# Performance work log

Hardware: AMD Instinct MI355X
Metric: run time of the kernel (lower is better)

## Reference

```python
import jax, jax.numpy as jnp
import numpy as np
from jax import lax

B, N, E, H = 512, 128, 256, 8
D = E // H
CLIP = 10.0
NEG = -1e9  # finite stand-in for -inf (backward-safe, math-identical after softmax)


def setup_inputs() -> dict:
    key = jax.random.key(0)
    ks = jax.random.split(key, 5)
    s = lambda k, shape: jax.random.normal(k, shape, jnp.float32) * 0.05
    return {
        "node_embeddings": jax.random.normal(ks[0], (B, N, E), jnp.float32),
        "Wqkv": s(ks[1], (E, 3 * E)), "bqkv": jnp.zeros((3 * E,), jnp.float32),
        "Wfix": s(ks[2], (E, E)), "bfix": jnp.zeros((E,), jnp.float32),
        "Wstep": s(ks[3], (2 * E, E)), "bstep": jnp.zeros((E,), jnp.float32),
        "Wmlp": s(ks[4], (E, E)), "bmlp": jnp.zeros((E,), jnp.float32),
    }


def reference(node_embeddings, Wqkv, bqkv, Wfix, bfix, Wstep, bstep, Wmlp, bmlp):
    scale = 1.0 / np.sqrt(D)
    graph_emb = node_embeddings.mean(axis=1)                       # (B,E)
    qkv = node_embeddings @ Wqkv + bqkv                            # (B,N,3E)
    k, v, logit_k = jnp.split(qkv, 3, axis=-1)
    kh = k.reshape(B, N, H, D).transpose(0, 2, 1, 3)               # (B,H,N,D)
    vh = v.reshape(B, N, H, D).transpose(0, 2, 1, 3)               # (B,H,N,D)
    fixed = graph_emb @ Wfix + bfix                                # (B,E)
    first = node_embeddings[:, 0, :]                               # (B,E)
    bidx = jnp.arange(B)

    def step(carry, _):
        current, visited, logp_sum = carry
        last = node_embeddings[bidx, current]                      # gather last action emb (B,E)
        q = fixed + (jnp.concatenate([first, last], axis=-1) @ Wstep + bstep)
        qh = q.reshape(B, H, D)                                    # single query per head
        attn = jnp.einsum('bhd,bhnd->bhn', qh, kh) * scale
        attn = jnp.where(visited[:, None, :], NEG, attn)
        attn = jax.nn.softmax(attn, axis=-1)
        ctx = jnp.einsum('bhn,bhnd->bhd', attn, vh).reshape(B, E)
        x = ctx @ Wmlp + bmlp                                      # (B,E)
        logits = jnp.einsum('be,bne->bn', x, logit_k) * scale      # (B,N)
        logits = jnp.tanh(logits) * CLIP
        logits = jnp.where(visited, NEG, logits)
        log_p = jax.nn.log_softmax(logits, axis=-1)
        action = jnp.argmax(log_p, axis=-1)                        # greedy decode
        chosen = jnp.take_along_axis(log_p, action[:, None], axis=1)[:, 0]
        visited = visited | jax.nn.one_hot(action, N, dtype=bool)
        return (action, visited, logp_sum + chosen), action

    visited0 = jnp.zeros((B, N), bool).at[:, 0].set(True)
    current0 = jnp.zeros((B,), jnp.int32)
    (_, _, logp_sum), seq = lax.scan(
        step, (current0, visited0, jnp.zeros((B,), jnp.float32)), None, length=N - 1)
    return logp_sum                                                # (B,) summed log-prob of tour
```

## Files before the change

kernel.cpp:

```cpp
#include <hip/hip_runtime.h>
#include <math.h>


#define B_ 512
#define N_ 128
#define E_ 256
#define H_ 8
#define D_ 32
#define NEG (-1.0e9f)
#define CLIPV 10.0f
#define SCALE 0.17677669529663688110f

template <int CTRL>
__device__ __forceinline__ float dpp_f(float x) {
  int r = __builtin_amdgcn_update_dpp(__float_as_int(x), __float_as_int(x),
                                      CTRL, 0xf, 0xf, false);
  return __int_as_float(r);
}
__device__ __forceinline__ float wred_max(float v) {
  v = fmaxf(v, dpp_f<0xB1>(v));
  v = fmaxf(v, dpp_f<0x4E>(v));
  v = fmaxf(v, dpp_f<0x124>(v));
  v = fmaxf(v, dpp_f<0x128>(v));
  v = fmaxf(v, __shfl_xor(v, 16));
  v = fmaxf(v, __shfl_xor(v, 32));
  return v;
}
__device__ __forceinline__ float wred_sum(float v) {
  v += dpp_f<0xB1>(v);
  v += dpp_f<0x4E>(v);
  v += dpp_f<0x124>(v);
  v += dpp_f<0x128>(v);
  v += __shfl_xor(v, 16);
  v += __shfl_xor(v, 32);
  return v;
}

__global__ void k0_prep(const float* __restrict__ Wqkv, const float* __restrict__ bqkv,
                        const float* __restrict__ Wmlp, const float* __restrict__ bmlp,
                        float* __restrict__ Wc, float* __restrict__ bc,
                        float* __restrict__ wc2, float* __restrict__ cconst) {
  int t = threadIdx.x;
  int blk = blockIdx.x;
  __shared__ float row_s[E_];
  if (blk < E_) {
    int g = blk;
    row_s[t] = Wqkv[g * 768 + 512 + t];
    __syncthreads();
    int f = t;
    const float4* wm4 = (const float4*)(Wmlp + f * E_);
    const float4* w34 = (const float4*)row_s;
    float acc = 0.f;
#pragma unroll 8
    for (int j = 0; j < E_ / 4; ++j) {
      float4 a = w34[j]; float4 bv = wm4[j];
      acc += a.x * bv.x + a.y * bv.y + a.z * bv.z + a.w * bv.w;
    }
    Wc[g * E_ + f] = acc;
  } else {
    int f = t;
    float a1 = 0.f, a2 = 0.f;
    for (int e = 0; e < E_; ++e) {
      a1 += bqkv[512 + e] * Wmlp[f * E_ + e];
      a2 += Wqkv[f * 768 + 512 + e] * bmlp[e];
    }
    bc[f] = a1;
    wc2[f] = a2;
    if (t == 0) {
      float c = 0.f;
      for (int e = 0; e < E_; ++e) c += bqkv[512 + e] * bmlp[e];
      *cconst = c;
    }
  }
}

__global__ __launch_bounds__(256, 2)
void k_gemm(const float* __restrict__ emb, const float* __restrict__ Wqkv,
            const float* __restrict__ bqkv,
            const float* __restrict__ Wc, const float* __restrict__ bc,
            float* __restrict__ kk_, float* __restrict__ vv_,
            float* __restrict__ lk2, int ncc, int tmask) {
  __shared__ float As[256 * 64];
  int t = threadIdx.x;
  int r0 = blockIdx.x * 64;
  {
    int m = t >> 2;
    int c0 = t & 3;
    const float4* e4 = (const float4*)emb;
#pragma unroll
    for (int p = 0; p < 16; ++p) {
      int c4 = c0 + p * 4;
      float4 a = e4[(size_t)(r0 + m) * 64 + c4];
      As[(c4 * 4 + 0) * 64 + m] = a.x;
      As[(c4 * 4 + 1) * 64 + m] = a.y;
      As[(c4 * 4 + 2) * 64 + m] = a.z;
      As[(c4 * 4 + 3) * 64 + m] = a.w;
    }
  }
  __syncthreads();
  int tx = t & 15, ty = t >> 4;
  const float4* As4 = (const float4*)As;
  for (int cc = 0; cc < ncc; ++cc) {
    const float* Bp; int ldb4; const float* bias; float* outp;
    int colbase = (cc & 1) * 128;
    switch (cc >> 1) {
      case 0:  Bp = Wqkv + colbase;          ldb4 = 192; bias = bqkv + colbase;       outp = kk_; break;
      case 1:  Bp = Wqkv + 256 + colbase;    ldb4 = 192; bias = bqkv + 256 + colbase; outp = vv_; break;
      default: Bp = Wc + colbase;            ldb4 = 64;  bias = bc + colbase;         outp = lk2; break;
    }
    const float4* B4 = (const float4*)Bp;
    float acc[4][8];
#pragma unroll
    for (int i = 0; i < 4; ++i)
#pragma unroll
      for (int j = 0; j < 8; ++j) acc[i][j] = 0.f;

#pragma unroll 4
    for (int kk = 0; kk < 256; ++kk) {
      float4 b0 = B4[kk * ldb4 + tx * 2];
      float4 b1 = B4[kk * ldb4 + tx * 2 + 1];
      float4 av = As4[kk * 16 + ty];
      float a_[4] = {av.x, av.y, av.z, av.w};
#pragma unroll
      for (int i = 0; i < 4; ++i) {
        acc[i][0] += a_[i] * b0.x; acc[i][1] += a_[i] * b0.y;
        acc[i][2] += a_[i] * b0.z; acc[i][3] += a_[i] * b0.w;
        acc[i][4] += a_[i] * b1.x; acc[i][5] += a_[i] * b1.y;
        acc[i][6] += a_[i] * b1.z; acc[i][7] += a_[i] * b1.w;
      }
    }
    float bj[8];
#pragma unroll
    for (int j = 0; j < 8; ++j) bj[j] = bias ? bias[tx * 8 + j] : 0.f;
    int tr = (tmask >> (cc >> 1)) & 1;
    if (!tr) {
#pragma unroll
      for (int i = 0; i < 4; ++i) {
        int row = r0 + ty * 4 + i;
        float4 o0 = make_float4(acc[i][0] + bj[0], acc[i][1] + bj[1], acc[i][2] + bj[2], acc[i][3] + bj[3]);
        float4 o1 = make_float4(acc[i][4] + bj[4], acc[i][5] + bj[5], acc[i][6] + bj[6], acc[i][7] + bj[7]);
        float4* o4 = (float4*)(outp + (size_t)row * 256 + colbase + tx * 8);
        o4[0] = o0; o4[1] = o1;
      }
    } else {
#pragma unroll
      for (int i = 0; i < 4; ++i) {
        int row = r0 + ty * 4 + i;
        int bb = row >> 7, nn = row & 127;
        float* op = outp + (size_t)bb * 32768 + nn;
#pragma unroll
        for (int j = 0; j < 8; ++j)
          op[(size_t)(colbase + tx * 8 + j) * 128] = acc[i][j] + bj[j];
      }
    }
  }
}

__global__ void k_qbase(const float* __restrict__ emb, const float* __restrict__ Wfix,
                        const float* __restrict__ bfix, const float* __restrict__ Wstep,
                        const float* __restrict__ bstep, float* __restrict__ qbase) {
  int b = blockIdx.x, t = threadIdx.x;
  __shared__ float ge[E_], fi[E_];
  const float* eb = emb + (size_t)b * N_ * E_;
  float s = 0.f;
#pragma unroll 8
  for (int n = 0; n < N_; ++n) s += eb[n * E_ + t];
  ge[t] = s * (1.0f / 128.0f);
  fi[t] = eb[t];
  __syncthreads();
  float acc = bfix[t] + bstep[t];
#pragma unroll 4
  for (int g = 0; g < E_; ++g)
    acc += ge[g] * Wfix[g * E_ + t] + fi[g] * Wstep[g * E_ + t];
  qbase[b * E_ + t] = acc;
}

__global__ void k_c(const float* __restrict__ emb, const float* __restrict__ wc2,
                    const float* __restrict__ cconst, float* __restrict__ cvec) {
  __shared__ float w[E_];
  int t = threadIdx.x;
  w[t] = wc2[t];
  __syncthreads();
  int row = blockIdx.x * 256 + t;
  const float4* e4 = (const float4*)(emb + (size_t)row * E_);
  const float4* w4 = (const float4*)w;
  float acc = 0.f;
#pragma unroll 8
  for (int j = 0; j < E_ / 4; ++j) {
    float4 a = e4[j], bv = w4[j];
    acc += a.x * bv.x + a.y * bv.y + a.z * bv.z + a.w * bv.w;
  }
  cvec[row] = acc + *cconst;
}

__global__ __launch_bounds__(512) __attribute__((amdgpu_waves_per_eu(2, 2)))
void k_roll(const float* __restrict__ emb, const float* __restrict__ Wstep,
            const float* __restrict__ kT, const float* __restrict__ vv_,
            const float* __restrict__ lkT,
            const float* __restrict__ qbase, const float* __restrict__ cvec,
            float* __restrict__ out) {
  int lt = threadIdx.x;
  int b = blockIdx.x;
  int h = lt >> 6;
  int j = lt & 63;

  __shared__ float sq_lds[128 * 260];
  __shared__ float work[6144];
  float* at_s  = work;
  float* ctx_s = work + 1024;
  float* zp    = work + 1280;

  {
    float* At = work;
    float* Bs = work + 2048;
    const float4* eb4 = (const float4*)(emb + (size_t)b * 32768);
    const float* W2 = Wstep + 65536;
    int n0 = (lt & 31) * 4;
    int e0 = (lt >> 5) * 16;
    float acc[4][16];
#pragma unroll
    for (int i = 0; i < 4; ++i)
#pragma unroll
      for (int jj = 0; jj < 16; ++jj) acc[i][jj] = 0.f;

    for (int gc = 0; gc < 16; ++gc) {
      {
        int n = lt & 127, q4g = lt >> 7;
        float4 a = eb4[n * 64 + gc * 4 + q4g];
        At[(q4g * 4 + 0) * 128 + n] = a.x;
        At[(q4g * 4 + 1) * 128 + n] = a.y;
        At[(q4g * 4 + 2) * 128 + n] = a.z;
        At[(q4g * 4 + 3) * 128 + n] = a.w;
      }
      {
        const float4* w4 = (const float4*)(W2 + gc * 16 * 256);
        ((float4*)Bs)[lt] = w4[lt];
        ((float4*)Bs)[lt + 512] = w4[lt + 512];
      }
      __syncthreads();
#pragma unroll
      for (int gi = 0; gi < 16; ++gi) {
        float4 a4 = *(const float4*)(At + gi * 128 + n0);
        const float4* bp = (const float4*)(Bs + gi * 256 + e0);
        float4 b0 = bp[0], b1 = bp[1], b2 = bp[2], b3 = bp[3];
        float av[4] = {a4.x, a4.y, a4.z, a4.w};
        float bv[16] = {b0.x, b0.y, b0.z, b0.w, b1.x, b1.y, b1.z, b1.w,
                        b2.x, b2.y, b2.z, b2.w, b3.x, b3.y, b3.z, b3.w};
#pragma unroll
        for (int i = 0; i < 4; ++i)
#pragma unroll
          for (int jj = 0; jj < 16; ++jj) acc[i][jj] += av[i] * bv[jj];
      }
      __syncthreads();
    }
    const float* qb = qbase + (size_t)b * 256;
    float qbr[16];
#pragma unroll
    for (int jj = 0; jj < 16; ++jj) qbr[jj] = qb[e0 + jj];
#pragma unroll
    for (int i = 0; i < 4; ++i)
#pragma unroll
      for (int jj = 0; jj < 16; ++jj)
        sq_lds[(n0 + i) * 260 + e0 + jj] = acc[i][jj] + qbr[jj];
  }
  __syncthreads();
  __builtin_amdgcn_sched_barrier(0);

  const float* kTb = kT + (size_t)b * 32768;
  const float* vb  = vv_ + (size_t)b * 32768;
  const float* lTb = lkT + (size_t)b * 32768;

  float k0r[32], k1r[32];
#pragma unroll
  for (int d = 0; d < 32; ++d) {
    k0r[d] = kTb[(h * 32 + d) * 128 + j];
    k1r[d] = kTb[(h * 32 + d) * 128 + j + 64];
  }
  int e_own = h * 32 + (j & 31), nh = j >> 5;
  float vr[64];
#pragma unroll
  for (int m = 0; m < 64; ++m) vr[m] = vb[(nh * 64 + m) * 256 + e_own];
  float l0r[32], l1r[32];
#pragma unroll
  for (int e = 0; e < 32; ++e) {
    l0r[e] = lTb[(h * 32 + e) * 128 + j];
    l1r[e] = lTb[(h * 32 + e) * 128 + j + 64];
  }
  float cv_lo = cvec[b * 128 + j];
  float cv_hi = cvec[b * 128 + j + 64];
  int vis_lo = (j == 0) ? 1 : 0, vis_hi = 0;
  int cur = 0;
  float lp = 0.f;

#pragma unroll 1
  for (int it = 0; it < N_ - 1; ++it) {
    const float4* q4 = (const float4*)(sq_lds + cur * 260 + h * 32);
    float sa0 = 0.f, sb0 = 0.f, sa1 = 0.f, sb1 = 0.f;
#pragma unroll
    for (int dd = 0; dd < 8; ++dd) {
      float4 qv = q4[dd];
      if (dd & 1) {
        sb0 += qv.x * k0r[dd * 4] + qv.y * k0r[dd * 4 + 1] + qv.z * k0r[dd * 4 + 2] + qv.w * k0r[dd * 4 + 3];
        sb1 += qv.x * k1r[dd * 4] + qv.y * k1r[dd * 4 + 1] + qv.z * k1r[dd * 4 + 2] + qv.w * k1r[dd * 4 + 3];
      } else {
        sa0 += qv.x * k0r[dd * 4] + qv.y * k0r[dd * 4 + 1] + qv.z * k0r[dd * 4 + 2] + qv.w * k0r[dd * 4 + 3];
        sa1 += qv.x * k1r[dd * 4] + qv.y * k1r[dd * 4 + 1] + qv.z * k1r[dd * 4 + 2] + qv.w * k1r[dd * 4 + 3];
      }
    }
    float slo = vis_lo ? NEG : (sa0 + sb0) * SCALE;
    float shi = vis_hi ? NEG : (sa1 + sb1) * SCALE;
    float m = wred_max(fmaxf(slo, shi));
    float elo = expf(slo - m), ehi = expf(shi - m);
    at_s[h * 128 + j] = elo;
    at_s[h * 128 + 64 + j] = ehi;
    float inv = 1.0f / wred_sum(elo + ehi);
    const float4* a4 = (const float4*)(at_s + h * 128 + nh * 64);
    float c0 = 0.f, c1 = 0.f;
#pragma unroll
    for (int mm = 0; mm < 16; ++mm) {
      float4 av = a4[mm];
      if (mm & 1)
        c1 += av.x * vr[mm * 4] + av.y * vr[mm * 4 + 1] + av.z * vr[mm * 4 + 2] + av.w * vr[mm * 4 + 3];
      else
        c0 += av.x * vr[mm * 4] + av.y * vr[mm * 4 + 1] + av.z * vr[mm * 4 + 2] + av.w * vr[mm * 4 + 3];
    }
    float c = c0 + c1;
    c += __shfl_xor(c, 32);
    c *= inv;
    if (j < 32) ctx_s[h * 32 + j] = c;
    const float4* cx4 = (const float4*)(ctx_s + h * 32);
    float z0a = 0.f, z0b = 0.f, z1a = 0.f, z1b = 0.f;
#pragma unroll
    for (int ee = 0; ee < 8; ++ee) {
      float4 cv = cx4[ee];
      if (ee & 1) {
        z0b += cv.x * l0r[ee * 4] + cv.y * l0r[ee * 4 + 1] + cv.z * l0r[ee * 4 + 2] + cv.w * l0r[ee * 4 + 3];
        z1b += cv.x * l1r[ee * 4] + cv.y * l1r[ee * 4 + 1] + cv.z * l1r[ee * 4 + 2] + cv.w * l1r[ee * 4 + 3];
      } else {
        z0a += cv.x * l0r[ee * 4] + cv.y * l0r[ee * 4 + 1] + cv.z * l0r[ee * 4 + 2] + cv.w * l0r[ee * 4 + 3];
        z1a += cv.x * l1r[ee * 4] + cv.y * l1r[ee * 4 + 1] + cv.z * l1r[ee * 4 + 2] + cv.w * l1r[ee * 4 + 3];
      }
    }
    float* zpw = zp + (it & 1) * 1024;
    zpw[h * 128 + j] = z0a + z0b;
    zpw[h * 128 + 64 + j] = z1a + z1b;
    __syncthreads();

    float zlo = cv_lo, zhi = cv_hi;
#pragma unroll
    for (int hh = 0; hh < 8; ++hh) {
      zlo += zpw[hh * 128 + j];
      zhi += zpw[hh * 128 + 64 + j];
    }
    float zmlo = vis_lo ? -1e30f : zlo;
    float zmhi = vis_hi ? -1e30f : zhi;
    float vmax = wred_max(fmaxf(zmlo, zmhi));
    unsigned long long blo = __ballot(zmlo == vmax);
    int action;
    if (blo) action = __ffsll((unsigned long long)blo) - 1;
    else     action = 63 + __ffsll((unsigned long long)__ballot(zmhi == vmax));
    float lmax = CLIPV * tanhf(vmax * SCALE);
    float tlo = vis_lo ? 0.f : expf(CLIPV * tanhf(zlo * SCALE) - 10.0f);
    float thi = vis_hi ? 0.f : expf(CLIPV * tanhf(zhi * SCALE) - 10.0f);
    float S = wred_sum(tlo + thi);
    lp += lmax - 10.0f - logf(S);
    cur = action;
    vis_lo |= (action == j);
    vis_hi |= (action == j + 64);
  }
  if (lt == 0) out[b] = lp;
}

extern "C" void kernel_launch(void* const* d_in, const int* in_sizes, int n_in,
                              void* d_out, int out_size, void* d_ws, size_t ws_size,
                              hipStream_t stream) {
  (void)in_sizes; (void)n_in; (void)out_size; (void)ws_size;
  const float* emb   = (const float*)d_in[0];
  const float* Wqkv  = (const float*)d_in[1];
  const float* bqkv  = (const float*)d_in[2];
  const float* Wfix  = (const float*)d_in[3];
  const float* bfix  = (const float*)d_in[4];
  const float* Wstep = (const float*)d_in[5];
  const float* bstep = (const float*)d_in[6];
  const float* Wmlp  = (const float*)d_in[7];
  const float* bmlp  = (const float*)d_in[8];
  float* out = (float*)d_out;
  float* ws = (float*)d_ws;

  const size_t NBE = (size_t)B_ * N_ * E_;
  float* kk_    = ws;
  float* vv_    = ws + NBE;
  float* lk2    = ws + 2 * NBE;
  float* qbase  = ws + 3 * NBE;
  float* cvec   = qbase + 131072;
  float* Wc     = cvec + 65536;
  float* bc     = Wc + 65536;
  float* wc2    = bc + 256;
  float* cconst = wc2 + 256;

  hipLaunchKernelGGL(k0_prep, dim3(257), dim3(256), 0, stream,
                     Wqkv, bqkv, Wmlp, bmlp, Wc, bc, wc2, cconst);
  hipLaunchKernelGGL(k_qbase, dim3(512), dim3(256), 0, stream,
                     emb, Wfix, bfix, Wstep, bstep, qbase);
  hipLaunchKernelGGL(k_c, dim3(256), dim3(256), 0, stream,
                     emb, wc2, cconst, cvec);
  hipLaunchKernelGGL(k_gemm, dim3(1024), dim3(256), 0, stream,
                     emb, Wqkv, bqkv, Wc, bc, kk_, vv_, lk2, 6, 0b101);
  hipLaunchKernelGGL(k_roll, dim3(512), dim3(512), 0, stream,
                     emb, Wstep, kk_, vv_, lk2, qbase, cvec, out);
}
```

Baseline: 1.368 ms.

## Split each head across two waves in rollout kernel with 1024-thread blocks

The rollout kernel doubles its block to 1024 threads, so each attention head is handled by two waves, each owning 64 of the 128 nodes. The softmax becomes a split-softmax: each wave writes its partial max, sum and context to LDS, and these are merged after an extra barrier per step. The point is to halve per-thread register arrays and serial work on the critical sequential path. The cost is an added __syncthreads per iteration, redundant exp and merge work, and removal of the waves_per_eu hint, which may change register allocation and occupancy.

New measurement: 1.549 ms. 1.13x slower.

```diff
diff --git a/kernel.cpp b/kernel.cpp
--- a/kernel.cpp
+++ b/kernel.cpp
@@ -193,7 +193,7 @@
   cvec[row] = acc + *cconst;
 }
 
-__global__ __launch_bounds__(512) __attribute__((amdgpu_waves_per_eu(2, 2)))
+__global__ __launch_bounds__(1024)
 void k_roll(const float* __restrict__ emb, const float* __restrict__ Wstep,
             const float* __restrict__ kT, const float* __restrict__ vv_,
             const float* __restrict__ lkT,
@@ -201,14 +201,17 @@
             float* __restrict__ out) {
   int lt = threadIdx.x;
   int b = blockIdx.x;
-  int h = lt >> 6;
+  int w = lt >> 6;
   int j = lt & 63;
+  int h = w >> 1;
+  int u = w & 1;
 
   __shared__ float sq_lds[128 * 260];
   __shared__ float work[6144];
-  float* at_s  = work;
-  float* ctx_s = work + 1024;
-  float* zp    = work + 1280;
+  float* at_s = work;
+  float* mS_s = work + 1024;
+  float* cxp2 = work + 1056;
+  float* zp_s = work + 1568;
 
   {
     float* At = work;
@@ -216,15 +219,15 @@
     const float4* eb4 = (const float4*)(emb + (size_t)b * 32768);
     const float* W2 = Wstep + 65536;
     int n0 = (lt & 31) * 4;
-    int e0 = (lt >> 5) * 16;
-    float acc[4][16];
+    int e0 = (lt >> 5) * 8;
+    float acc[4][8];
 #pragma unroll
     for (int i = 0; i < 4; ++i)
 #pragma unroll
-      for (int jj = 0; jj < 16; ++jj) acc[i][jj] = 0.f;
+      for (int jj = 0; jj < 8; ++jj) acc[i][jj] = 0.f;
 
     for (int gc = 0; gc < 16; ++gc) {
-      {
+      if (lt < 512) {
         int n = lt & 127, q4g = lt >> 7;
         float4 a = eb4[n * 64 + gc * 4 + q4g];
         At[(q4g * 4 + 0) * 128 + n] = a.x;
@@ -235,32 +238,30 @@
       {
         const float4* w4 = (const float4*)(W2 + gc * 16 * 256);
         ((float4*)Bs)[lt] = w4[lt];
-        ((float4*)Bs)[lt + 512] = w4[lt + 512];
       }
       __syncthreads();
 #pragma unroll
       for (int gi = 0; gi < 16; ++gi) {
         float4 a4 = *(const float4*)(At + gi * 128 + n0);
         const float4* bp = (const float4*)(Bs + gi * 256 + e0);
-        float4 b0 = bp[0], b1 = bp[1], b2 = bp[2], b3 = bp[3];
+        float4 b0 = bp[0], b1 = bp[1];
         float av[4] = {a4.x, a4.y, a4.z, a4.w};
-        float bv[16] = {b0.x, b0.y, b0.z, b0.w, b1.x, b1.y, b1.z, b1.w,
-                        b2.x, b2.y, b2.z, b2.w, b3.x, b3.y, b3.z, b3.w};
+        float bv[8] = {b0.x, b0.y, b0.z, b0.w, b1.x, b1.y, b1.z, b1.w};
 #pragma unroll
         for (int i = 0; i < 4; ++i)
 #pragma unroll
-          for (int jj = 0; jj < 16; ++jj) acc[i][jj] += av[i] * bv[jj];
+          for (int jj = 0; jj < 8; ++jj) acc[i][jj] += av[i] * bv[jj];
       }
       __syncthreads();
     }
     const float* qb = qbase + (size_t)b * 256;
-    float qbr[16];
-#pragma unroll
-    for (int jj = 0; jj < 16; ++jj) qbr[jj] = qb[e0 + jj];
+    float qbr[8];
+#pragma unroll
+    for (int jj = 0; jj < 8; ++jj) qbr[jj] = qb[e0 + jj];
 #pragma unroll
     for (int i = 0; i < 4; ++i)
 #pragma unroll
-      for (int jj = 0; jj < 16; ++jj)
+      for (int jj = 0; jj < 8; ++jj)
         sq_lds[(n0 + i) * 260 + e0 + jj] = acc[i][jj] + qbr[jj];
   }
   __syncthreads();
@@ -269,25 +270,24 @@
   const float* kTb = kT + (size_t)b * 32768;
   const float* vb  = vv_ + (size_t)b * 32768;
   const float* lTb = lkT + (size_t)b * 32768;
-
-  float k0r[32], k1r[32];
-#pragma unroll
-  for (int d = 0; d < 32; ++d) {
-    k0r[d] = kTb[(h * 32 + d) * 128 + j];
-    k1r[d] = kTb[(h * 32 + d) * 128 + j + 64];
-  }
-  int e_own = h * 32 + (j & 31), nh = j >> 5;
-  float vr[64];
-#pragma unroll
-  for (int m = 0; m < 64; ++m) vr[m] = vb[(nh * 64 + m) * 256 + e_own];
-  float l0r[32], l1r[32];
-#pragma unroll
-  for (int e = 0; e < 32; ++e) {
-    l0r[e] = lTb[(h * 32 + e) * 128 + j];
-    l1r[e] = lTb[(h * 32 + e) * 128 + j + 64];
-  }
+  int nob = u * 64;
+
+  float kr[32];
+#pragma unroll
+  for (int d = 0; d < 32; ++d) kr[d] = kTb[(h * 32 + d) * 128 + nob + j];
+
+  int e_own = h * 32 + (j & 31);
+  int nb = u * 2 + (j >> 5);
+  float vr[32];
+#pragma unroll
+  for (int m = 0; m < 32; ++m) vr[m] = vb[(nb * 32 + m) * 256 + e_own];
+
+  float lr[32];
+#pragma unroll
+  for (int e = 0; e < 32; ++e) lr[e] = lTb[(h * 32 + e) * 128 + nob + j];
+
   float cv_lo = cvec[b * 128 + j];
-  float cv_hi = cvec[b * 128 + j + 64];
+  float cv_hi = cvec[b * 128 + 64 + j];
   int vis_lo = (j == 0) ? 1 : 0, vis_hi = 0;
   int cur = 0;
   float lp = 0.f;
@@ -295,62 +295,62 @@
 #pragma unroll 1
   for (int it = 0; it < N_ - 1; ++it) {
     const float4* q4 = (const float4*)(sq_lds + cur * 260 + h * 32);
-    float sa0 = 0.f, sb0 = 0.f, sa1 = 0.f, sb1 = 0.f;
+    float sa = 0.f, sb = 0.f;
 #pragma unroll
     for (int dd = 0; dd < 8; ++dd) {
       float4 qv = q4[dd];
-      if (dd & 1) {
-        sb0 += qv.x * k0r[dd * 4] + qv.y * k0r[dd * 4 + 1] + qv.z * k0r[dd * 4 + 2] + qv.w * k0r[dd * 4 + 3];
-        sb1 += qv.x * k1r[dd * 4] + qv.y * k1r[dd * 4 + 1] + qv.z * k1r[dd * 4 + 2] + qv.w * k1r[dd * 4 + 3];
-      } else {
-        sa0 += qv.x * k0r[dd * 4] + qv.y * k0r[dd * 4 + 1] + qv.z * k0r[dd * 4 + 2] + qv.w * k0r[dd * 4 + 3];
-        sa1 += qv.x * k1r[dd * 4] + qv.y * k1r[dd * 4 + 1] + qv.z * k1r[dd * 4 + 2] + qv.w * k1r[dd * 4 + 3];
-      }
-    }
-    float slo = vis_lo ? NEG : (sa0 + sb0) * SCALE;
-    float shi = vis_hi ? NEG : (sa1 + sb1) * SCALE;
-    float m = wred_max(fmaxf(slo, shi));
-    float elo = expf(slo - m), ehi = expf(shi - m);
-    at_s[h * 128 + j] = elo;
-    at_s[h * 128 + 64 + j] = ehi;
-    float inv = 1.0f / wred_sum(elo + ehi);
-    const float4* a4 = (const float4*)(at_s + h * 128 + nh * 64);
-    float c0 = 0.f, c1 = 0.f;
-#pragma unroll
-    for (int mm = 0; mm < 16; ++mm) {
+      float t = qv.x * kr[dd * 4] + qv.y * kr[dd * 4 + 1] +
+                qv.z * kr[dd * 4 + 2] + qv.w * kr[dd * 4 + 3];
+      if (dd & 1) sb += t; else sa += t;
+    }
+    int vis_own = u ? vis_hi : vis_lo;
+    float sv = vis_own ? NEG : (sa + sb) * SCALE;
+    float mw = wred_max(sv);
+    float ev = expf(sv - mw);
+    float Sw = wred_sum(ev);
+    at_s[w * 64 + j] = ev;
+    if (j == 0) { mS_s[w * 2] = mw; mS_s[w * 2 + 1] = Sw; }
+
+    const float4* a4 = (const float4*)(at_s + w * 64 + (j >> 5) * 32);
+    float p0 = 0.f, p1 = 0.f;
+#pragma unroll
+    for (int mm = 0; mm < 8; ++mm) {
       float4 av = a4[mm];
-      if (mm & 1)
-        c1 += av.x * vr[mm * 4] + av.y * vr[mm * 4 + 1] + av.z * vr[mm * 4 + 2] + av.w * vr[mm * 4 + 3];
-      else
-        c0 += av.x * vr[mm * 4] + av.y * vr[mm * 4 + 1] + av.z * vr[mm * 4 + 2] + av.w * vr[mm * 4 + 3];
-    }
-    float c = c0 + c1;
-    c += __shfl_xor(c, 32);
-    c *= inv;
-    if (j < 32) ctx_s[h * 32 + j] = c;
-    const float4* cx4 = (const float4*)(ctx_s + h * 32);
-    float z0a = 0.f, z0b = 0.f, z1a = 0.f, z1b = 0.f;
+      float t = av.x * vr[mm * 4] + av.y * vr[mm * 4 + 1] +
+                av.z * vr[mm * 4 + 2] + av.w * vr[mm * 4 + 3];
+      if (mm & 1) p1 += t; else p0 += t;
+    }
+    float p = p0 + p1;
+    float ph = p + __shfl_xor(p, 32);
+    if (j < 32) cxp2[w * 32 + j] = ph;
+    __syncthreads();
+
+    float m0 = mS_s[4 * h], S0 = mS_s[4 * h + 1];
+    float m1 = mS_s[4 * h + 2], S1 = mS_s[4 * h + 3];
+    float mh = fmaxf(m0, m1);
+    float a0 = expf(m0 - mh), a1 = expf(m1 - mh);
+    float inv = 1.0f / (S0 * a0 + S1 * a1);
+    const float4* c0 = (const float4*)(cxp2 + (2 * h) * 32);
+    const float4* c1 = (const float4*)(cxp2 + (2 * h + 1) * 32);
+    float za0 = 0.f, za1 = 0.f, zb0 = 0.f, zb1 = 0.f;
 #pragma unroll
     for (int ee = 0; ee < 8; ++ee) {
-      float4 cv = cx4[ee];
-      if (ee & 1) {
-        z0b += cv.x * l0r[ee * 4] + cv.y * l0r[ee * 4 + 1] + cv.z * l0r[ee * 4 + 2] + cv.w * l0r[ee * 4 + 3];
-        z1b += cv.x * l1r[ee * 4] + cv.y * l1r[ee * 4 + 1] + cv.z * l1r[ee * 4 + 2] + cv.w * l1r[ee * 4 + 3];
-      } else {
-        z0a += cv.x * l0r[ee * 4] + cv.y * l0r[ee * 4 + 1] + cv.z * l0r[ee * 4 + 2] + cv.w * l0r[ee * 4 + 3];
-        z1a += cv.x * l1r[ee * 4] + cv.y * l1r[ee * 4 + 1] + cv.z * l1r[ee * 4 + 2] + cv.w * l1r[ee * 4 + 3];
-      }
-    }
-    float* zpw = zp + (it & 1) * 1024;
-    zpw[h * 128 + j] = z0a + z0b;
-    zpw[h * 128 + 64 + j] = z1a + z1b;
+      float4 cv0 = c0[ee], cv1 = c1[ee];
+      float t0 = cv0.x * lr[ee * 4] + cv0.y * lr[ee * 4 + 1] +
+                 cv0.z * lr[ee * 4 + 2] + cv0.w * lr[ee * 4 + 3];
+      float t1 = cv1.x * lr[ee * 4] + cv1.y * lr[ee * 4 + 1] +
+                 cv1.z * lr[ee * 4 + 2] + cv1.w * lr[ee * 4 + 3];
+      if (ee & 1) { za1 += t0; zb1 += t1; } else { za0 += t0; zb0 += t1; }
+    }
+    float z = (a0 * (za0 + za1) + a1 * (zb0 + zb1)) * inv;
+    zp_s[h * 128 + nob + j] = z;
     __syncthreads();
 
     float zlo = cv_lo, zhi = cv_hi;
 #pragma unroll
     for (int hh = 0; hh < 8; ++hh) {
-      zlo += zpw[hh * 128 + j];
-      zhi += zpw[hh * 128 + 64 + j];
+      zlo += zp_s[hh * 128 + j];
+      zhi += zp_s[hh * 128 + 64 + j];
     }
     float zmlo = vis_lo ? -1e30f : zlo;
     float zmhi = vis_hi ? -1e30f : zhi;
@@ -359,11 +359,13 @@
     int action;
     if (blo) action = __ffsll((unsigned long long)blo) - 1;
     else     action = 63 + __ffsll((unsigned long long)__ballot(zmhi == vmax));
-    float lmax = CLIPV * tanhf(vmax * SCALE);
-    float tlo = vis_lo ? 0.f : expf(CLIPV * tanhf(zlo * SCALE) - 10.0f);
-    float thi = vis_hi ? 0.f : expf(CLIPV * tanhf(zhi * SCALE) - 10.0f);
-    float S = wred_sum(tlo + thi);
-    lp += lmax - 10.0f - logf(S);
+    if (w == 0) {
+      float lmax = CLIPV * tanhf(vmax * SCALE);
+      float tlo = vis_lo ? 0.f : expf(CLIPV * tanhf(zlo * SCALE) - 10.0f);
+      float thi = vis_hi ? 0.f : expf(CLIPV * tanhf(zhi * SCALE) - 10.0f);
+      float S = wred_sum(tlo + thi);
+      lp += lmax - 10.0f - logf(S);
+    }
     cur = action;
     vis_lo |= (action == j);
     vis_hi |= (action == j + 64);
@@ -406,6 +408,6 @@
                      emb, wc2, cconst, cvec);
   hipLaunchKernelGGL(k_gemm, dim3(1024), dim3(256), 0, stream,
                      emb, Wqkv, bqkv, Wc, bc, kk_, vv_, lk2, 6, 0b101);
-  hipLaunchKernelGGL(k_roll, dim3(512), dim3(512), 0, stream,
+  hipLaunchKernelGGL(k_roll, dim3(512), dim3(1024), 0, stream,
                      emb, Wstep, kk_, vv_, lk2, qbase, cvec, out);
 }
```

## Use packed FMA, DPP row reductions, swizzled partial layout, single-wave logprob

Applied to the files above, without the earlier changes.

Converts the per-step dot products (q·k, attn·v, ctx·logit_k) to v_pk_fma_f32 on register pairs so each instruction does two FMAs. Wave reductions now use DPP row broadcasts plus a readlane instead of two cross-lane shuffles. The per-head partial logits are stored node-major with an XOR swizzle, so each lane reads its eight partials as two float4 LDS loads. Only wave 0 computes the tanh/exp/log log-probability, removing work the other seven waves duplicated. Inline asm and register-pinning barriers can limit compiler scheduling and may raise register pressure.

New measurement: 1.201 ms. 12.2% less time.

```diff
diff --git a/kernel.cpp b/kernel.cpp
--- a/kernel.cpp
+++ b/kernel.cpp
@@ -11,29 +11,41 @@
 #define CLIPV 10.0f
 #define SCALE 0.17677669529663688110f
 
+typedef float v2f __attribute__((ext_vector_type(2)));
+
+__device__ __forceinline__ void pkfma(v2f& acc, v2f a, v2f b) {
+  asm("v_pk_fma_f32 %0, %1, %2, %0" : "+v"(acc) : "v"(a), "v"(b));
+}
+
 template <int CTRL>
 __device__ __forceinline__ float dpp_f(float x) {
   int r = __builtin_amdgcn_update_dpp(__float_as_int(x), __float_as_int(x),
                                       CTRL, 0xf, 0xf, false);
   return __int_as_float(r);
 }
+template <int CTRL, int RM>
+__device__ __forceinline__ float dpp_mv(float x, float idv) {
+  int r = __builtin_amdgcn_update_dpp(__float_as_int(idv), __float_as_int(x),
+                                      CTRL, RM, 0xf, false);
+  return __int_as_float(r);
+}
 __device__ __forceinline__ float wred_max(float v) {
   v = fmaxf(v, dpp_f<0xB1>(v));
   v = fmaxf(v, dpp_f<0x4E>(v));
   v = fmaxf(v, dpp_f<0x124>(v));
   v = fmaxf(v, dpp_f<0x128>(v));
-  v = fmaxf(v, __shfl_xor(v, 16));
-  v = fmaxf(v, __shfl_xor(v, 32));
-  return v;
+  v = fmaxf(v, dpp_mv<0x142, 0xa>(v, -1e38f));
+  v = fmaxf(v, dpp_mv<0x143, 0xc>(v, -1e38f));
+  return __int_as_float(__builtin_amdgcn_readlane(__float_as_int(v), 63));
 }
 __device__ __forceinline__ float wred_sum(float v) {
   v += dpp_f<0xB1>(v);
   v += dpp_f<0x4E>(v);
   v += dpp_f<0x124>(v);
   v += dpp_f<0x128>(v);
-  v += __shfl_xor(v, 16);
-  v += __shfl_xor(v, 32);
-  return v;
+  v += dpp_mv<0x142, 0xa>(v, 0.0f);
+  v += dpp_mv<0x143, 0xc>(v, 0.0f);
+  return __int_as_float(__builtin_amdgcn_readlane(__float_as_int(v), 63));
 }
 
 __global__ void k0_prep(const float* __restrict__ Wqkv, const float* __restrict__ bqkv,
@@ -193,7 +205,7 @@
   cvec[row] = acc + *cconst;
 }
 
-__global__ __launch_bounds__(512) __attribute__((amdgpu_waves_per_eu(2, 2)))
+__global__ __attribute__((amdgpu_flat_work_group_size(512, 512), amdgpu_waves_per_eu(2, 2)))
 void k_roll(const float* __restrict__ emb, const float* __restrict__ Wstep,
             const float* __restrict__ kT, const float* __restrict__ vv_,
             const float* __restrict__ lkT,
@@ -270,88 +282,90 @@
   const float* vb  = vv_ + (size_t)b * 32768;
   const float* lTb = lkT + (size_t)b * 32768;
 
-  float k0r[32], k1r[32];
-#pragma unroll
-  for (int d = 0; d < 32; ++d) {
-    k0r[d] = kTb[(h * 32 + d) * 128 + j];
-    k1r[d] = kTb[(h * 32 + d) * 128 + j + 64];
+  v2f k0p[16], k1p[16];
+#pragma unroll
+  for (int d = 0; d < 16; ++d) {
+    k0p[d] = (v2f){kTb[(h * 32 + 2 * d) * 128 + j],     kTb[(h * 32 + 2 * d + 1) * 128 + j]};
+    k1p[d] = (v2f){kTb[(h * 32 + 2 * d) * 128 + j + 64], kTb[(h * 32 + 2 * d + 1) * 128 + j + 64]};
+    asm("" : "+v"(k0p[d]));
+    asm("" : "+v"(k1p[d]));
   }
   int e_own = h * 32 + (j & 31), nh = j >> 5;
-  float vr[64];
-#pragma unroll
-  for (int m = 0; m < 64; ++m) vr[m] = vb[(nh * 64 + m) * 256 + e_own];
-  float l0r[32], l1r[32];
-#pragma unroll
-  for (int e = 0; e < 32; ++e) {
-    l0r[e] = lTb[(h * 32 + e) * 128 + j];
-    l1r[e] = lTb[(h * 32 + e) * 128 + j + 64];
+  v2f vp[32];
+#pragma unroll
+  for (int m = 0; m < 32; ++m) {
+    vp[m] = (v2f){vb[(nh * 64 + 2 * m) * 256 + e_own], vb[(nh * 64 + 2 * m + 1) * 256 + e_own]};
+    asm("" : "+v"(vp[m]));
+  }
+  v2f l0p[16], l1p[16];
+#pragma unroll
+  for (int e = 0; e < 16; ++e) {
+    l0p[e] = (v2f){lTb[(h * 32 + 2 * e) * 128 + j],      lTb[(h * 32 + 2 * e + 1) * 128 + j]};
+    l1p[e] = (v2f){lTb[(h * 32 + 2 * e) * 128 + j + 64], lTb[(h * 32 + 2 * e + 1) * 128 + j + 64]};
+    asm("" : "+v"(l0p[e]));
+    asm("" : "+v"(l1p[e]));
   }
   float cv_lo = cvec[b * 128 + j];
   float cv_hi = cvec[b * 128 + j + 64];
   int vis_lo = (j == 0) ? 1 : 0, vis_hi = 0;
   int cur = 0;
   float lp = 0.f;
+  int swz = (j >> 2) & 7;
 
 #pragma unroll 1
   for (int it = 0; it < N_ - 1; ++it) {
     const float4* q4 = (const float4*)(sq_lds + cur * 260 + h * 32);
-    float sa0 = 0.f, sb0 = 0.f, sa1 = 0.f, sb1 = 0.f;
+    v2f s00 = {0.f, 0.f}, s01 = {0.f, 0.f}, s10 = {0.f, 0.f}, s11 = {0.f, 0.f};
 #pragma unroll
     for (int dd = 0; dd < 8; ++dd) {
       float4 qv = q4[dd];
-      if (dd & 1) {
-        sb0 += qv.x * k0r[dd * 4] + qv.y * k0r[dd * 4 + 1] + qv.z * k0r[dd * 4 + 2] + qv.w * k0r[dd * 4 + 3];
-        sb1 += qv.x * k1r[dd * 4] + qv.y * k1r[dd * 4 + 1] + qv.z * k1r[dd * 4 + 2] + qv.w * k1r[dd * 4 + 3];
-      } else {
-        sa0 += qv.x * k0r[dd * 4] + qv.y * k0r[dd * 4 + 1] + qv.z * k0r[dd * 4 + 2] + qv.w * k0r[dd * 4 + 3];
-        sa1 += qv.x * k1r[dd * 4] + qv.y * k1r[dd * 4 + 1] + qv.z * k1r[dd * 4 + 2] + qv.w * k1r[dd * 4 + 3];
-      }
-    }
-    float slo = vis_lo ? NEG : (sa0 + sb0) * SCALE;
-    float shi = vis_hi ? NEG : (sa1 + sb1) * SCALE;
+      v2f qa = {qv.x, qv.y}, qb = {qv.z, qv.w};
+      pkfma(s00, qa, k0p[2 * dd]);
+      pkfma(s01, qb, k0p[2 * dd + 1]);
+      pkfma(s10, qa, k1p[2 * dd]);
+      pkfma(s11, qb, k1p[2 * dd + 1]);
+    }
+    float slo = vis_lo ? NEG : ((s00.x + s00.y) + (s01.x + s01.y)) * SCALE;
+    float shi = vis_hi ? NEG : ((s10.x + s10.y) + (s11.x + s11.y)) * SCALE;
     float m = wred_max(fmaxf(slo, shi));
     float elo = expf(slo - m), ehi = expf(shi - m);
     at_s[h * 128 + j] = elo;
     at_s[h * 128 + 64 + j] = ehi;
     float inv = 1.0f / wred_sum(elo + ehi);
     const float4* a4 = (const float4*)(at_s + h * 128 + nh * 64);
-    float c0 = 0.f, c1 = 0.f;
+    v2f c0 = {0.f, 0.f}, c1 = {0.f, 0.f};
 #pragma unroll
     for (int mm = 0; mm < 16; ++mm) {
       float4 av = a4[mm];
-      if (mm & 1)
-        c1 += av.x * vr[mm * 4] + av.y * vr[mm * 4 + 1] + av.z * vr[mm * 4 + 2] + av.w * vr[mm * 4 + 3];
-      else
-        c0 += av.x * vr[mm * 4] + av.y * vr[mm * 4 + 1] + av.z * vr[mm * 4 + 2] + av.w * vr[mm * 4 + 3];
-    }
-    float c = c0 + c1;
+      v2f aa = {av.x, av.y}, ab = {av.z, av.w};
+      pkfma(c0, aa, vp[2 * mm]);
+      pkfma(c1, ab, vp[2 * mm + 1]);
+    }
+    float c = (c0.x + c0.y) + (c1.x + c1.y);
     c += __shfl_xor(c, 32);
     c *= inv;
     if (j < 32) ctx_s[h * 32 + j] = c;
     const float4* cx4 = (const float4*)(ctx_s + h * 32);
-    float z0a = 0.f, z0b = 0.f, z1a = 0.f, z1b = 0.f;
+    v2f z00 = {0.f, 0.f}, z01 = {0.f, 0.f}, z10 = {0.f, 0.f}, z11 = {0.f, 0.f};
 #pragma unroll
     for (int ee = 0; ee < 8; ++ee) {
       float4 cv = cx4[ee];
-      if (ee & 1) {
-        z0b += cv.x * l0r[ee * 4] + cv.y * l0r[ee * 4 + 1] + cv.z * l0r[ee * 4 + 2] + cv.w * l0r[ee * 4 + 3];
-        z1b += cv.x * l1r[ee * 4] + cv.y * l1r[ee * 4 + 1] + cv.z * l1r[ee * 4 + 2] + cv.w * l1r[ee * 4 + 3];
-      } else {
-        z0a += cv.x * l0r[ee * 4] + cv.y * l0r[ee * 4 + 1] + cv.z * l0r[ee * 4 + 2] + cv.w * l0r[ee * 4 + 3];
-        z1a += cv.x * l1r[ee * 4] + cv.y * l1r[ee * 4 + 1] + cv.z * l1r[ee * 4 + 2] + cv.w * l1r[ee * 4 + 3];
-      }
+      v2f ca = {cv.x, cv.y}, cb = {cv.z, cv.w};
+      pkfma(z00, ca, l0p[2 * ee]);
+      pkfma(z01, cb, l0p[2 * ee + 1]);
+      pkfma(z10, ca, l1p[2 * ee]);
+      pkfma(z11, cb, l1p[2 * ee + 1]);
     }
     float* zpw = zp + (it & 1) * 1024;
-    zpw[h * 128 + j] = z0a + z0b;
-    zpw[h * 128 + 64 + j] = z1a + z1b;
+    zpw[j * 8 + (h ^ swz)]        = (z00.x + z00.y) + (z01.x + z01.y);
+    zpw[(j + 64) * 8 + (h ^ swz)] = (z10.x + z10.y) + (z11.x + z11.y);
     __syncthreads();
 
-    float zlo = cv_lo, zhi = cv_hi;
-#pragma unroll
-    for (int hh = 0; hh < 8; ++hh) {
-      zlo += zpw[hh * 128 + j];
-      zhi += zpw[hh * 128 + 64 + j];
-    }
+    const float4* zr0 = (const float4*)(zpw + j * 8);
+    const float4* zr1 = (const float4*)(zpw + (j + 64) * 8);
+    float4 za = zr0[0], zb = zr0[1], zc = zr1[0], zd = zr1[1];
+    float zlo = cv_lo + ((za.x + za.y) + (za.z + za.w)) + ((zb.x + zb.y) + (zb.z + zb.w));
+    float zhi = cv_hi + ((zc.x + zc.y) + (zc.z + zc.w)) + ((zd.x + zd.y) + (zd.z + zd.w));
     float zmlo = vis_lo ? -1e30f : zlo;
     float zmhi = vis_hi ? -1e30f : zhi;
     float vmax = wred_max(fmaxf(zmlo, zmhi));
@@ -359,11 +373,13 @@
     int action;
     if (blo) action = __ffsll((unsigned long long)blo) - 1;
     else     action = 63 + __ffsll((unsigned long long)__ballot(zmhi == vmax));
-    float lmax = CLIPV * tanhf(vmax * SCALE);
-    float tlo = vis_lo ? 0.f : expf(CLIPV * tanhf(zlo * SCALE) - 10.0f);
-    float thi = vis_hi ? 0.f : expf(CLIPV * tanhf(zhi * SCALE) - 10.0f);
-    float S = wred_sum(tlo + thi);
-    lp += lmax - 10.0f - logf(S);
+    if (h == 0) {
+      float lmax = CLIPV * tanhf(vmax * SCALE);
+      float tlo = vis_lo ? 0.f : expf(CLIPV * tanhf(zlo * SCALE) - 10.0f);
+      float thi = vis_hi ? 0.f : expf(CLIPV * tanhf(zhi * SCALE) - 10.0f);
+      float S = wred_sum(tlo + thi);
+      lp += lmax - 10.0f - logf(S);
+    }
     cur = action;
     vis_lo |= (action == j);
     vis_hi |= (action == j + 64);
```
